# Kernel optimization log

Hardware: AMD Instinct MI355X
Metric: run time of the kernel (lower is better)

Reference implementation:

```python
import jax, jax.numpy as jnp
import numpy as np

INPUT_SHAPE = (4, 8, 8, 4)   # factorization of input_size=1024
RANK = 16                    # uniform TR rank; tr_ranks_line = [16]*9
NODES = 8                    # input_num=4, output_num=4
INPUT_NUM = 4


def setup_inputs() -> dict:
    key = jax.random.key(0)
    ks = jax.random.split(key, 10)
    B = 1024
    # node shapes from generate_node_shapes() with the chosen factorization
    node_shapes = [(256, 4), (16, 128), (16, 128), (16, 64),
                   (64, 16), (128, 16), (128, 16), (4, 256)]
    inp = {"x": jax.random.normal(ks[0], (B, 1024), dtype=jnp.float32)}
    for i, sh in enumerate(node_shapes):
        # kaiming_normal_(fan_in, linear) ~ N(0, sqrt(2/fan_in)) gain differences ignored for
        # correctness baseline; plain scaled normal init
        fan_in = sh[1]
        inp[f"node{i}"] = jax.random.normal(ks[i + 1], sh, dtype=jnp.float32) * np.float32(np.sqrt(1.0 / fan_in))
    inp["bias"] = jnp.zeros((1024,), dtype=jnp.float32)
    return inp


def _tensor_contract(x, weights):
    B = x.shape[0]
    # view(-1, *input_shape) then reverse the input mode axes (permute 0, n, n-1, ..., 1)
    res = x.reshape(B, *INPUT_SHAPE).transpose(0, 4, 3, 2, 1)  # (B, m3, m2, m1, m0)
    for i, W in enumerate(weights):
        wr = W.shape[1]
        if i == 0:
            res = res.reshape(-1, wr) @ W.T                 # (B*rest, r0*r1)
            res = res.reshape(B, -1, RANK).transpose(0, 2, 1)  # (B, r0, rest*r1)
        elif i < NODES - 1:
            # both remaining input nodes and all-but-last output nodes are a flat GEMM
            res = res.reshape(-1, wr) @ W.T
        else:
            # last node: (B, r_last_right, -1, r_last_left) -> swap ring ranks around middle
            res = res.reshape(B, RANK, -1, RANK).transpose(0, 2, 1, 3)
            res = res.reshape(-1, wr) @ W.T                 # (B*rest, m_last)
            res = res.reshape(B, -1)                         # (B, output_size)
    return res


def reference(x, node0, node1, node2, node3, node4, node5, node6, node7, bias):
    weights = [node0, node1, node2, node3, node4, node5, node6, node7]
    res = _tensor_contract(x, weights)
    return res + bias
```

## Files before the change

kernel.cpp:

```cpp
#include <hip/hip_runtime.h>
#include <hip/hip_bf16.h>

typedef __attribute__((ext_vector_type(8))) short bf16x8;
typedef __attribute__((ext_vector_type(4))) float f32x4;
typedef unsigned short u16;

static __device__ __forceinline__ u16 f2bf(float f) {
  unsigned u = __builtin_bit_cast(unsigned, f);
  return (u16)((u + 0x7fffu + ((u >> 16) & 1u)) >> 16);
}

__global__ __launch_bounds__(256) void trl_p1(
    const float* __restrict__ W0, const float* __restrict__ W1,
    const float* __restrict__ W2, const float* __restrict__ W3,
    const float* __restrict__ W4, const float* __restrict__ W5,
    const float* __restrict__ W6, const float* __restrict__ W7,
    const float* __restrict__ x,
    float* __restrict__ T1, float* __restrict__ V1,
    float* __restrict__ U1, float* __restrict__ V2,
    u16* __restrict__ xb) {
  const int gid = blockIdx.x * 256 + threadIdx.x;
  if (gid < 8192) {
    int i0 = gid & 3, i1 = (gid >> 2) & 7, j1 = (gid >> 5) & 15, r1 = gid >> 9;
    float s = 0.f;
#pragma unroll
    for (int r0 = 0; r0 < 16; ++r0)
      s += W1[j1 * 128 + i1 * 16 + r0] * W0[(r0 * 16 + r1) * 4 + i0];
    T1[gid] = s;
  } else if (gid < 16384) {
    int g = gid - 8192;
    int j1 = g & 15, i2 = (g >> 4) & 7, i3 = (g >> 7) & 3, j3 = g >> 9;
    float s = 0.f;
#pragma unroll
    for (int j2 = 0; j2 < 16; ++j2)
      s += W3[j3 * 64 + i3 * 16 + j2] * W2[j2 * 128 + i2 * 16 + j1];
    V1[g] = s;
  } else if (gid < 24576) {
    int g = gid - 16384;
    int j3 = g & 15, j5 = (g >> 4) & 127, kh = g >> 11;
    float s = 0.f;
#pragma unroll
    for (int kl = 0; kl < 16; ++kl)
      s += W5[j5 * 16 + kl] * W4[(kh * 16 + kl) * 16 + j3];
    U1[g] = s;
  } else {
    int g = gid - 24576;
    int j5l = g & 15, j6h = (g >> 4) & 7, r1 = (g >> 7) & 15, m7 = g >> 11;
    float s = 0.f;
#pragma unroll
    for (int d = 0; d < 16; ++d)
      s += W7[m7 * 256 + r1 * 16 + d] * W6[(j6h * 16 + d) * 16 + j5l];
    V2[g] = s;
  }
#pragma unroll
  for (int q = 0; q < 4; ++q) {
    const int c = gid + 65536 * q;
    const float4 v = reinterpret_cast<const float4*>(x)[c];
    ushort4 o4;
    o4.x = f2bf(v.x); o4.y = f2bf(v.y); o4.z = f2bf(v.z); o4.w = f2bf(v.w);
    reinterpret_cast<ushort4*>(xb)[c] = o4;
  }
}

__global__ __launch_bounds__(256) void trl_p2(
    const float* __restrict__ T1, const float* __restrict__ V1,
    const float* __restrict__ U1, const float* __restrict__ V2,
    u16* __restrict__ Apre, u16* __restrict__ Bmat) {
  const int gid = blockIdx.x * 256 + threadIdx.x;
  if (gid < 65536) {
    const int p = gid >> 8, irest = gid & 255;
    const int r1 = p >> 4, j3 = p & 15;
    const int i1 = irest >> 5, i2 = (irest >> 2) & 7, i3 = irest & 3;
    float4 a = make_float4(0.f, 0.f, 0.f, 0.f);
#pragma unroll
    for (int j1 = 0; j1 < 16; ++j1) {
      const float w = V1[((j3 * 4 + i3) * 8 + i2) * 16 + j1];
      const float4 t = reinterpret_cast<const float4*>(T1)[(r1 * 16 + j1) * 8 + i1];
      a.x += w * t.x; a.y += w * t.y; a.z += w * t.z; a.w += w * t.w;
    }
    Apre[p * 1024 + 0 * 256 + irest] = f2bf(a.x);
    Apre[p * 1024 + 1 * 256 + irest] = f2bf(a.y);
    Apre[p * 1024 + 2 * 256 + irest] = f2bf(a.z);
    Apre[p * 1024 + 3 * 256 + irest] = f2bf(a.w);
  } else {
    const int t = gid - 65536;
    const int o = t >> 6, rem = t & 63;
    const int r1 = rem >> 2, jq = rem & 3;
    const int m7 = o & 3, j6h = (o >> 2) & 7, j5h = (o >> 5) & 7, kh = o >> 8;
    float4 a = make_float4(0.f, 0.f, 0.f, 0.f);
#pragma unroll
    for (int j5l = 0; j5l < 16; ++j5l) {
      const float w = V2[((m7 * 16 + r1) * 8 + j6h) * 16 + j5l];
      const float4 u = reinterpret_cast<const float4*>(U1)[(kh * 128 + j5h * 16 + j5l) * 4 + jq];
      a.x += w * u.x; a.y += w * u.y; a.z += w * u.z; a.w += w * u.w;
    }
    ushort4 o4;
    o4.x = f2bf(a.x); o4.y = f2bf(a.y); o4.z = f2bf(a.z); o4.w = f2bf(a.w);
    *reinterpret_cast<ushort4*>(&Bmat[o * 256 + r1 * 16 + jq * 4]) = o4;
  }
}

__global__ __launch_bounds__(256) void trl_g1(const u16* __restrict__ A,
                                              const u16* __restrict__ B,
                                              u16* __restrict__ C) {
  __shared__ float red[3][32 * 33];
  const int tid = threadIdx.x;
  const int wave = tid >> 6, lane = tid & 63;
  const int l15 = lane & 15, l4 = lane >> 4;
  const int m0 = blockIdx.y * 32, n0 = blockIdx.x * 32;
  const int kbase = wave * 256;

  f32x4 acc[2][2] = {};
#pragma unroll
  for (int ks = 0; ks < 8; ++ks) {
    const int k = kbase + ks * 32 + l4 * 8;
    const bf16x8 a0 = *(const bf16x8*)&A[(size_t)(m0 + l15) * 1024 + k];
    const bf16x8 a1 = *(const bf16x8*)&A[(size_t)(m0 + 16 + l15) * 1024 + k];
    const bf16x8 b0 = *(const bf16x8*)&B[(size_t)(n0 + l15) * 1024 + k];
    const bf16x8 b1 = *(const bf16x8*)&B[(size_t)(n0 + 16 + l15) * 1024 + k];
    acc[0][0] = __builtin_amdgcn_mfma_f32_16x16x32_bf16(a0, b0, acc[0][0], 0, 0, 0);
    acc[0][1] = __builtin_amdgcn_mfma_f32_16x16x32_bf16(a0, b1, acc[0][1], 0, 0, 0);
    acc[1][0] = __builtin_amdgcn_mfma_f32_16x16x32_bf16(a1, b0, acc[1][0], 0, 0, 0);
    acc[1][1] = __builtin_amdgcn_mfma_f32_16x16x32_bf16(a1, b1, acc[1][1], 0, 0, 0);
  }

  if (wave > 0) {
#pragma unroll
    for (int fm = 0; fm < 2; ++fm)
#pragma unroll
      for (int fn = 0; fn < 2; ++fn)
#pragma unroll
        for (int r = 0; r < 4; ++r)
          red[wave - 1][(fm * 16 + l4 * 4 + r) * 33 + fn * 16 + l15] = acc[fm][fn][r];
  }
  __syncthreads();
  if (wave == 0) {
#pragma unroll
    for (int fm = 0; fm < 2; ++fm)
#pragma unroll
      for (int fn = 0; fn < 2; ++fn)
#pragma unroll
        for (int r = 0; r < 4; ++r) {
          const int row = fm * 16 + l4 * 4 + r, col = fn * 16 + l15;
          float s = acc[fm][fn][r] + red[0][row * 33 + col] + red[1][row * 33 + col] +
                    red[2][row * 33 + col];
          C[(size_t)(m0 + row) * 256 + n0 + col] = f2bf(s);
        }
  }
}

__global__ __launch_bounds__(256) void trl_g2(const u16* __restrict__ A,
                                              const u16* __restrict__ B,
                                              const float* __restrict__ bias,
                                              float* __restrict__ out) {
  const int tid = threadIdx.x;
  const int wave = tid >> 6, lane = tid & 63;
  const int l15 = lane & 15, l4 = lane >> 4;
  const int tile = blockIdx.x * 4 + wave;
  const int m0 = (tile >> 5) * 32, n0 = (tile & 31) * 32;

  f32x4 acc[2][2] = {};
#pragma unroll
  for (int ks = 0; ks < 8; ++ks) {
    const int k = ks * 32 + l4 * 8;
    const bf16x8 a0 = *(const bf16x8*)&A[(size_t)(m0 + l15) * 256 + k];
    const bf16x8 a1 = *(const bf16x8*)&A[(size_t)(m0 + 16 + l15) * 256 + k];
    const bf16x8 b0 = *(const bf16x8*)&B[(size_t)(n0 + l15) * 256 + k];
    const bf16x8 b1 = *(const bf16x8*)&B[(size_t)(n0 + 16 + l15) * 256 + k];
    acc[0][0] = __builtin_amdgcn_mfma_f32_16x16x32_bf16(a0, b0, acc[0][0], 0, 0, 0);
    acc[0][1] = __builtin_amdgcn_mfma_f32_16x16x32_bf16(a0, b1, acc[0][1], 0, 0, 0);
    acc[1][0] = __builtin_amdgcn_mfma_f32_16x16x32_bf16(a1, b0, acc[1][0], 0, 0, 0);
    acc[1][1] = __builtin_amdgcn_mfma_f32_16x16x32_bf16(a1, b1, acc[1][1], 0, 0, 0);
  }

#pragma unroll
  for (int fn = 0; fn < 2; ++fn) {
    const int gc = n0 + fn * 16 + l15;
    const float bv = bias[gc];
#pragma unroll
    for (int fm = 0; fm < 2; ++fm)
#pragma unroll
      for (int r = 0; r < 4; ++r) {
        const int gr = m0 + fm * 16 + l4 * 4 + r;
        out[(size_t)gr * 1024 + gc] = acc[fm][fn][r] + bv;
      }
  }
}

extern "C" void kernel_launch(void* const* d_in, const int* in_sizes, int n_in,
                              void* d_out, int out_size, void* d_ws, size_t ws_size,
                              hipStream_t stream) {
  const float* x  = (const float*)d_in[0];
  const float* W0 = (const float*)d_in[1];
  const float* W1 = (const float*)d_in[2];
  const float* W2 = (const float*)d_in[3];
  const float* W3 = (const float*)d_in[4];
  const float* W4 = (const float*)d_in[5];
  const float* W5 = (const float*)d_in[6];
  const float* W6 = (const float*)d_in[7];
  const float* W7 = (const float*)d_in[8];
  const float* bias = (const float*)d_in[9];

  char* ws = (char*)d_ws;
  float* T1 = (float*)(ws + (0 << 10));
  float* V1 = (float*)(ws + (32 << 10));
  float* U1 = (float*)(ws + (64 << 10));
  float* V2 = (float*)(ws + (96 << 10));
  u16* Apre = (u16*)(ws + (128 << 10));
  u16* Bmat = (u16*)(ws + (640 << 10));
  u16* xb   = (u16*)(ws + (1152 << 10));
  u16* Cb   = (u16*)(ws + (3200 << 10));
  float* outp = (float*)d_out;

  trl_p1<<<256, 256, 0, stream>>>(W0, W1, W2, W3, W4, W5, W6, W7, x, T1, V1, U1, V2, xb);
  trl_p2<<<512, 256, 0, stream>>>(T1, V1, U1, V2, Apre, Bmat);
  trl_g1<<<dim3(8, 32), 256, 0, stream>>>(xb, Apre, Cb);
  trl_g2<<<256, 256, 0, stream>>>(Cb, Bmat, bias, outp);
}
```

Before: 25.78 us.

## Fuse weight prep into one kernel and both GEMMs into one kernel

```diff
diff --git a/kernel.cpp b/kernel.cpp
--- a/kernel.cpp
+++ b/kernel.cpp
@@ -10,180 +10,156 @@
   return (u16)((u + 0x7fffu + ((u >> 16) & 1u)) >> 16);
 }
 
-__global__ __launch_bounds__(256) void trl_p1(
+__global__ __launch_bounds__(256) void trl_w(
     const float* __restrict__ W0, const float* __restrict__ W1,
     const float* __restrict__ W2, const float* __restrict__ W3,
     const float* __restrict__ W4, const float* __restrict__ W5,
     const float* __restrict__ W6, const float* __restrict__ W7,
-    const float* __restrict__ x,
-    float* __restrict__ T1, float* __restrict__ V1,
-    float* __restrict__ U1, float* __restrict__ V2,
-    u16* __restrict__ xb) {
-  const int gid = blockIdx.x * 256 + threadIdx.x;
-  if (gid < 8192) {
-    int i0 = gid & 3, i1 = (gid >> 2) & 7, j1 = (gid >> 5) & 15, r1 = gid >> 9;
-    float s = 0.f;
+    u16* __restrict__ Apre, u16* __restrict__ Bmat) {
+  __shared__ float S1[512];
+  __shared__ float S2[4096];
+  const int tid = threadIdx.x;
+  const int b = blockIdx.x;
+  if (b < 64) {
+    const int r1 = b >> 2;
+    const int j3base = (b & 3) << 2;
 #pragma unroll
-    for (int r0 = 0; r0 < 16; ++r0)
-      s += W1[j1 * 128 + i1 * 16 + r0] * W0[(r0 * 16 + r1) * 4 + i0];
-    T1[gid] = s;
-  } else if (gid < 16384) {
-    int g = gid - 8192;
-    int j1 = g & 15, i2 = (g >> 4) & 7, i3 = (g >> 7) & 3, j3 = g >> 9;
-    float s = 0.f;
+    for (int e0 = 0; e0 < 512; e0 += 256) {
+      const int e = e0 + tid;
+      const int i0 = e & 3, i1 = (e >> 2) & 7, j1 = e >> 5;
+      float s = 0.f;
 #pragma unroll
-    for (int j2 = 0; j2 < 16; ++j2)
-      s += W3[j3 * 64 + i3 * 16 + j2] * W2[j2 * 128 + i2 * 16 + j1];
-    V1[g] = s;
-  } else if (gid < 24576) {
-    int g = gid - 16384;
-    int j3 = g & 15, j5 = (g >> 4) & 127, kh = g >> 11;
-    float s = 0.f;
+      for (int r0 = 0; r0 < 16; ++r0)
+        s += W1[j1 * 128 + i1 * 16 + r0] * W0[(r0 * 16 + r1) * 4 + i0];
+      S1[e] = s;
+    }
 #pragma unroll
-    for (int kl = 0; kl < 16; ++kl)
-      s += W5[j5 * 16 + kl] * W4[(kh * 16 + kl) * 16 + j3];
-    U1[g] = s;
+    for (int e0 = 0; e0 < 2048; e0 += 256) {
+      const int e = e0 + tid;
+      const int i3 = e & 3, pd = (e >> 2) & 3, j1 = (e >> 4) & 15, i2 = e >> 8;
+      float s = 0.f;
+#pragma unroll
+      for (int j2 = 0; j2 < 16; ++j2)
+        s += W3[(j3base + pd) * 64 + i3 * 16 + j2] * W2[j2 * 128 + i2 * 16 + j1];
+      S2[e] = s;
+    }
+    __syncthreads();
+    const int i0 = tid & 3, i1 = (tid >> 2) & 7, i2 = tid >> 5;
+#pragma unroll
+    for (int pd = 0; pd < 4; ++pd) {
+      float a0 = 0.f, a1 = 0.f, a2 = 0.f, a3 = 0.f;
+#pragma unroll
+      for (int j1 = 0; j1 < 16; ++j1) {
+        const float t = S1[j1 * 32 + i1 * 4 + i0];
+        const float4 v = *(const float4*)&S2[i2 * 256 + j1 * 16 + pd * 4];
+        a0 += t * v.x; a1 += t * v.y; a2 += t * v.z; a3 += t * v.w;
+      }
+      ushort4 o4;
+      o4.x = f2bf(a0); o4.y = f2bf(a1); o4.z = f2bf(a2); o4.w = f2bf(a3);
+      *(ushort4*)&Apre[(size_t)(4 * b + pd) * 1024 + i0 * 256 + i1 * 32 + i2 * 4] = o4;
+    }
   } else {
-    int g = gid - 24576;
-    int j5l = g & 15, j6h = (g >> 4) & 7, r1 = (g >> 7) & 15, m7 = g >> 11;
-    float s = 0.f;
+    const int c = b - 64;
+    const int kh = c >> 4, j5h = (c >> 1) & 7, j6hbase = (c & 1) << 2;
+    {
+      const int j5l = tid >> 4, j3 = tid & 15;
+      float s = 0.f;
 #pragma unroll
-    for (int d = 0; d < 16; ++d)
-      s += W7[m7 * 256 + r1 * 16 + d] * W6[(j6h * 16 + d) * 16 + j5l];
-    V2[g] = s;
-  }
+      for (int kl = 0; kl < 16; ++kl)
+        s += W5[(j5h * 16 + j5l) * 16 + kl] * W4[(kh * 16 + kl) * 16 + j3];
+      S1[tid] = s;
+    }
 #pragma unroll
-  for (int q = 0; q < 4; ++q) {
-    const int c = gid + 65536 * q;
-    const float4 v = reinterpret_cast<const float4*>(x)[c];
-    ushort4 o4;
-    o4.x = f2bf(v.x); o4.y = f2bf(v.y); o4.z = f2bf(v.z); o4.w = f2bf(v.w);
-    reinterpret_cast<ushort4*>(xb)[c] = o4;
+    for (int e0 = 0; e0 < 4096; e0 += 256) {
+      const int e = e0 + tid;
+      const int j5l = e & 15, j6hd = (e >> 4) & 3, r1 = (e >> 6) & 15, m7 = e >> 10;
+      float s = 0.f;
+#pragma unroll
+      for (int d = 0; d < 16; ++d)
+        s += W7[m7 * 256 + r1 * 16 + d] * W6[((j6hbase + j6hd) * 16 + d) * 16 + j5l];
+      S2[e] = s;
+    }
+    __syncthreads();
+    const int r1 = (tid >> 2) & 15, j3q = tid & 3;
+#pragma unroll
+    for (int qq = 0; qq < 4; ++qq) {
+      const int od = qq * 4 + (tid >> 6);
+      const int m7 = od & 3, j6hd = od >> 2;
+      float a0 = 0.f, a1 = 0.f, a2 = 0.f, a3 = 0.f;
+#pragma unroll
+      for (int j5l = 0; j5l < 16; ++j5l) {
+        const float w = S2[((m7 * 16 + r1) * 4 + j6hd) * 16 + j5l];
+        const float4 u = *(const float4*)&S1[j5l * 16 + j3q * 4];
+        a0 += w * u.x; a1 += w * u.y; a2 += w * u.z; a3 += w * u.w;
+      }
+      ushort4 o4;
+      o4.x = f2bf(a0); o4.y = f2bf(a1); o4.z = f2bf(a2); o4.w = f2bf(a3);
+      *(ushort4*)&Bmat[(size_t)(16 * c + od) * 256 + r1 * 16 + j3q * 4] = o4;
+    }
   }
 }
 
-__global__ __launch_bounds__(256) void trl_p2(
-    const float* __restrict__ T1, const float* __restrict__ V1,
-    const float* __restrict__ U1, const float* __restrict__ V2,
-    u16* __restrict__ Apre, u16* __restrict__ Bmat) {
-  const int gid = blockIdx.x * 256 + threadIdx.x;
-  if (gid < 65536) {
-    const int p = gid >> 8, irest = gid & 255;
-    const int r1 = p >> 4, j3 = p & 15;
-    const int i1 = irest >> 5, i2 = (irest >> 2) & 7, i3 = irest & 3;
-    float4 a = make_float4(0.f, 0.f, 0.f, 0.f);
-#pragma unroll
-    for (int j1 = 0; j1 < 16; ++j1) {
-      const float w = V1[((j3 * 4 + i3) * 8 + i2) * 16 + j1];
-      const float4 t = reinterpret_cast<const float4*>(T1)[(r1 * 16 + j1) * 8 + i1];
-      a.x += w * t.x; a.y += w * t.y; a.z += w * t.z; a.w += w * t.w;
-    }
-    Apre[p * 1024 + 0 * 256 + irest] = f2bf(a.x);
-    Apre[p * 1024 + 1 * 256 + irest] = f2bf(a.y);
-    Apre[p * 1024 + 2 * 256 + irest] = f2bf(a.z);
-    Apre[p * 1024 + 3 * 256 + irest] = f2bf(a.w);
-  } else {
-    const int t = gid - 65536;
-    const int o = t >> 6, rem = t & 63;
-    const int r1 = rem >> 2, jq = rem & 3;
-    const int m7 = o & 3, j6h = (o >> 2) & 7, j5h = (o >> 5) & 7, kh = o >> 8;
-    float4 a = make_float4(0.f, 0.f, 0.f, 0.f);
-#pragma unroll
-    for (int j5l = 0; j5l < 16; ++j5l) {
-      const float w = V2[((m7 * 16 + r1) * 8 + j6h) * 16 + j5l];
-      const float4 u = reinterpret_cast<const float4*>(U1)[(kh * 128 + j5h * 16 + j5l) * 4 + jq];
-      a.x += w * u.x; a.y += w * u.y; a.z += w * u.z; a.w += w * u.w;
-    }
-    ushort4 o4;
-    o4.x = f2bf(a.x); o4.y = f2bf(a.y); o4.z = f2bf(a.z); o4.w = f2bf(a.w);
-    *reinterpret_cast<ushort4*>(&Bmat[o * 256 + r1 * 16 + jq * 4]) = o4;
-  }
-}
-
-__global__ __launch_bounds__(256) void trl_g1(const u16* __restrict__ A,
-                                              const u16* __restrict__ B,
-                                              u16* __restrict__ C) {
-  __shared__ float red[3][32 * 33];
+__global__ __launch_bounds__(256) void trl_g(const float* __restrict__ x,
+                                             const u16* __restrict__ Apre,
+                                             const u16* __restrict__ Bmat,
+                                             const float* __restrict__ bias,
+                                             float* __restrict__ out) {
+  __shared__ u16 Cbs[16 * 256];
   const int tid = threadIdx.x;
   const int wave = tid >> 6, lane = tid & 63;
   const int l15 = lane & 15, l4 = lane >> 4;
-  const int m0 = blockIdx.y * 32, n0 = blockIdx.x * 32;
-  const int kbase = wave * 256;
+  const int m0 = blockIdx.x * 16;
 
-  f32x4 acc[2][2] = {};
+  f32x4 acc1[4] = {};
+  {
+    const float* xrow = x + (size_t)(m0 + l15) * 1024;
+#pragma unroll 4
+    for (int kb = 0; kb < 32; ++kb) {
+      const int k = kb * 32 + l4 * 8;
+      const float4 f0 = *(const float4*)&xrow[k];
+      const float4 f1 = *(const float4*)&xrow[k + 4];
+      bf16x8 af;
+      af[0] = (short)f2bf(f0.x); af[1] = (short)f2bf(f0.y);
+      af[2] = (short)f2bf(f0.z); af[3] = (short)f2bf(f0.w);
+      af[4] = (short)f2bf(f1.x); af[5] = (short)f2bf(f1.y);
+      af[6] = (short)f2bf(f1.z); af[7] = (short)f2bf(f1.w);
 #pragma unroll
-  for (int ks = 0; ks < 8; ++ks) {
-    const int k = kbase + ks * 32 + l4 * 8;
-    const bf16x8 a0 = *(const bf16x8*)&A[(size_t)(m0 + l15) * 1024 + k];
-    const bf16x8 a1 = *(const bf16x8*)&A[(size_t)(m0 + 16 + l15) * 1024 + k];
-    const bf16x8 b0 = *(const bf16x8*)&B[(size_t)(n0 + l15) * 1024 + k];
-    const bf16x8 b1 = *(const bf16x8*)&B[(size_t)(n0 + 16 + l15) * 1024 + k];
-    acc[0][0] = __builtin_amdgcn_mfma_f32_16x16x32_bf16(a0, b0, acc[0][0], 0, 0, 0);
-    acc[0][1] = __builtin_amdgcn_mfma_f32_16x16x32_bf16(a0, b1, acc[0][1], 0, 0, 0);
-    acc[1][0] = __builtin_amdgcn_mfma_f32_16x16x32_bf16(a1, b0, acc[1][0], 0, 0, 0);
-    acc[1][1] = __builtin_amdgcn_mfma_f32_16x16x32_bf16(a1, b1, acc[1][1], 0, 0, 0);
+      for (int nt = 0; nt < 4; ++nt) {
+        const bf16x8 bf = *(const bf16x8*)&Apre[(size_t)(wave * 64 + nt * 16 + l15) * 1024 + k];
+        acc1[nt] = __builtin_amdgcn_mfma_f32_16x16x32_bf16(af, bf, acc1[nt], 0, 0, 0);
+      }
+    }
   }
-
-  if (wave > 0) {
 #pragma unroll
-    for (int fm = 0; fm < 2; ++fm)
+  for (int nt = 0; nt < 4; ++nt) {
+    const int col = wave * 64 + nt * 16 + l15;
 #pragma unroll
-      for (int fn = 0; fn < 2; ++fn)
-#pragma unroll
-        for (int r = 0; r < 4; ++r)
-          red[wave - 1][(fm * 16 + l4 * 4 + r) * 33 + fn * 16 + l15] = acc[fm][fn][r];
+    for (int r = 0; r < 4; ++r) {
+      const int row = l4 * 4 + r;
+      Cbs[row * 256 + ((((col >> 3) ^ (row & 7)) << 3) | (col & 7))] = f2bf(acc1[nt][r]);
+    }
   }
   __syncthreads();
-  if (wave == 0) {
+
+  f32x4 acc2[16] = {};
+#pragma unroll 2
+  for (int kb = 0; kb < 8; ++kb) {
+    const int g = kb * 4 + l4;
+    const bf16x8 af = *(const bf16x8*)&Cbs[l15 * 256 + ((g ^ (l15 & 7)) << 3)];
 #pragma unroll
-    for (int fm = 0; fm < 2; ++fm)
+    for (int nt = 0; nt < 16; ++nt) {
+      const bf16x8 bf =
+          *(const bf16x8*)&Bmat[(size_t)(wave * 256 + nt * 16 + l15) * 256 + kb * 32 + l4 * 8];
+      acc2[nt] = __builtin_amdgcn_mfma_f32_16x16x32_bf16(af, bf, acc2[nt], 0, 0, 0);
+    }
+  }
 #pragma unroll
-      for (int fn = 0; fn < 2; ++fn)
+  for (int nt = 0; nt < 16; ++nt) {
+    const int col = wave * 256 + nt * 16 + l15;
+    const float bv = bias[col];
 #pragma unroll
-        for (int r = 0; r < 4; ++r) {
-          const int row = fm * 16 + l4 * 4 + r, col = fn * 16 + l15;
-          float s = acc[fm][fn][r] + red[0][row * 33 + col] + red[1][row * 33 + col] +
-                    red[2][row * 33 + col];
-          C[(size_t)(m0 + row) * 256 + n0 + col] = f2bf(s);
-        }
-  }
-}
-
-__global__ __launch_bounds__(256) void trl_g2(const u16* __restrict__ A,
-                                              const u16* __restrict__ B,
-                                              const float* __restrict__ bias,
-                                              float* __restrict__ out) {
-  const int tid = threadIdx.x;
-  const int wave = tid >> 6, lane = tid & 63;
-  const int l15 = lane & 15, l4 = lane >> 4;
-  const int tile = blockIdx.x * 4 + wave;
-  const int m0 = (tile >> 5) * 32, n0 = (tile & 31) * 32;
-
-  f32x4 acc[2][2] = {};
-#pragma unroll
-  for (int ks = 0; ks < 8; ++ks) {
-    const int k = ks * 32 + l4 * 8;
-    const bf16x8 a0 = *(const bf16x8*)&A[(size_t)(m0 + l15) * 256 + k];
-    const bf16x8 a1 = *(const bf16x8*)&A[(size_t)(m0 + 16 + l15) * 256 + k];
-    const bf16x8 b0 = *(const bf16x8*)&B[(size_t)(n0 + l15) * 256 + k];
-    const bf16x8 b1 = *(const bf16x8*)&B[(size_t)(n0 + 16 + l15) * 256 + k];
-    acc[0][0] = __builtin_amdgcn_mfma_f32_16x16x32_bf16(a0, b0, acc[0][0], 0, 0, 0);
-    acc[0][1] = __builtin_amdgcn_mfma_f32_16x16x32_bf16(a0, b1, acc[0][1], 0, 0, 0);
-    acc[1][0] = __builtin_amdgcn_mfma_f32_16x16x32_bf16(a1, b0, acc[1][0], 0, 0, 0);
-    acc[1][1] = __builtin_amdgcn_mfma_f32_16x16x32_bf16(a1, b1, acc[1][1], 0, 0, 0);
-  }
-
-#pragma unroll
-  for (int fn = 0; fn < 2; ++fn) {
-    const int gc = n0 + fn * 16 + l15;
-    const float bv = bias[gc];
-#pragma unroll
-    for (int fm = 0; fm < 2; ++fm)
-#pragma unroll
-      for (int r = 0; r < 4; ++r) {
-        const int gr = m0 + fm * 16 + l4 * 4 + r;
-        out[(size_t)gr * 1024 + gc] = acc[fm][fn][r] + bv;
-      }
+    for (int r = 0; r < 4; ++r)
+      out[(size_t)(m0 + l4 * 4 + r) * 1024 + col] = acc2[nt][r] + bv;
   }
 }
 
@@ -202,18 +178,10 @@
   const float* bias = (const float*)d_in[9];
 
   char* ws = (char*)d_ws;
-  float* T1 = (float*)(ws + (0 << 10));
-  float* V1 = (float*)(ws + (32 << 10));
-  float* U1 = (float*)(ws + (64 << 10));
-  float* V2 = (float*)(ws + (96 << 10));
-  u16* Apre = (u16*)(ws + (128 << 10));
-  u16* Bmat = (u16*)(ws + (640 << 10));
-  u16* xb   = (u16*)(ws + (1152 << 10));
-  u16* Cb   = (u16*)(ws + (3200 << 10));
+  u16* Apre = (u16*)(ws);
+  u16* Bmat = (u16*)(ws + (512 << 10));
   float* outp = (float*)d_out;
 
-  trl_p1<<<256, 256, 0, stream>>>(W0, W1, W2, W3, W4, W5, W6, W7, x, T1, V1, U1, V2, xb);
-  trl_p2<<<512, 256, 0, stream>>>(T1, V1, U1, V2, Apre, Bmat);
-  trl_g1<<<dim3(8, 32), 256, 0, stream>>>(xb, Apre, Cb);
-  trl_g2<<<256, 256, 0, stream>>>(Cb, Bmat, bias, outp);
+  trl_w<<<128, 256, 0, stream>>>(W0, W1, W2, W3, W4, W5, W6, W7, Apre, Bmat);
+  trl_g<<<64, 256, 0, stream>>>(x, Apre, Bmat, bias, outp);
 }
```

Result: slower. 72.78 us (+182.3%).

## Fuse weight-contraction prologues into GEMM kernels, building B tiles in LDS

Applied to the files above, without the earlier changes.

```diff
diff --git a/kernel.cpp b/kernel.cpp
--- a/kernel.cpp
+++ b/kernel.cpp
@@ -10,120 +10,95 @@
   return (u16)((u + 0x7fffu + ((u >> 16) & 1u)) >> 16);
 }
 
-__global__ __launch_bounds__(256) void trl_p1(
+__global__ __launch_bounds__(256) void trl_g1(
+    const float* __restrict__ x,
     const float* __restrict__ W0, const float* __restrict__ W1,
     const float* __restrict__ W2, const float* __restrict__ W3,
-    const float* __restrict__ W4, const float* __restrict__ W5,
-    const float* __restrict__ W6, const float* __restrict__ W7,
-    const float* __restrict__ x,
-    float* __restrict__ T1, float* __restrict__ V1,
-    float* __restrict__ U1, float* __restrict__ V2,
-    u16* __restrict__ xb) {
-  const int gid = blockIdx.x * 256 + threadIdx.x;
-  if (gid < 8192) {
-    int i0 = gid & 3, i1 = (gid >> 2) & 7, j1 = (gid >> 5) & 15, r1 = gid >> 9;
+    u16* __restrict__ Cb) {
+  __shared__ float S_T1[1024];
+  __shared__ float S_V1[8192];
+  __shared__ u16 Bs[128 * 32 * 8];
+  __shared__ float red[3][32 * 33];
+  const int tid = threadIdx.x;
+  const int n0 = blockIdx.x * 32;
+  const int m0 = blockIdx.y * 32;
+  const int r1a = n0 >> 4;
+
+  for (int k = 0; k < 4; ++k) {
+    const int e = tid + 256 * k;
+    const int i0 = e & 3, i1 = (e >> 2) & 7, j1 = (e >> 5) & 15, rr = e >> 9;
     float s = 0.f;
 #pragma unroll
     for (int r0 = 0; r0 < 16; ++r0)
-      s += W1[j1 * 128 + i1 * 16 + r0] * W0[(r0 * 16 + r1) * 4 + i0];
-    T1[gid] = s;
-  } else if (gid < 16384) {
-    int g = gid - 8192;
-    int j1 = g & 15, i2 = (g >> 4) & 7, i3 = (g >> 7) & 3, j3 = g >> 9;
+      s += W1[j1 * 128 + i1 * 16 + r0] * W0[(r0 * 16 + r1a + rr) * 4 + i0];
+    S_T1[e] = s;
+  }
+  for (int k = 0; k < 32; ++k) {
+    const int e = tid + 256 * k;
+    const int j1 = e & 15, i2 = (e >> 4) & 7, i3 = (e >> 7) & 3, j3 = e >> 9;
     float s = 0.f;
 #pragma unroll
     for (int j2 = 0; j2 < 16; ++j2)
       s += W3[j3 * 64 + i3 * 16 + j2] * W2[j2 * 128 + i2 * 16 + j1];
-    V1[g] = s;
-  } else if (gid < 24576) {
-    int g = gid - 16384;
-    int j3 = g & 15, j5 = (g >> 4) & 127, kh = g >> 11;
-    float s = 0.f;
-#pragma unroll
-    for (int kl = 0; kl < 16; ++kl)
-      s += W5[j5 * 16 + kl] * W4[(kh * 16 + kl) * 16 + j3];
-    U1[g] = s;
-  } else {
-    int g = gid - 24576;
-    int j5l = g & 15, j6h = (g >> 4) & 7, r1 = (g >> 7) & 15, m7 = g >> 11;
-    float s = 0.f;
-#pragma unroll
-    for (int d = 0; d < 16; ++d)
-      s += W7[m7 * 256 + r1 * 16 + d] * W6[(j6h * 16 + d) * 16 + j5l];
-    V2[g] = s;
-  }
-#pragma unroll
-  for (int q = 0; q < 4; ++q) {
-    const int c = gid + 65536 * q;
-    const float4 v = reinterpret_cast<const float4*>(x)[c];
-    ushort4 o4;
-    o4.x = f2bf(v.x); o4.y = f2bf(v.y); o4.z = f2bf(v.z); o4.w = f2bf(v.w);
-    reinterpret_cast<ushort4*>(xb)[c] = o4;
-  }
-}
-
-__global__ __launch_bounds__(256) void trl_p2(
-    const float* __restrict__ T1, const float* __restrict__ V1,
-    const float* __restrict__ U1, const float* __restrict__ V2,
-    u16* __restrict__ Apre, u16* __restrict__ Bmat) {
-  const int gid = blockIdx.x * 256 + threadIdx.x;
-  if (gid < 65536) {
-    const int p = gid >> 8, irest = gid & 255;
-    const int r1 = p >> 4, j3 = p & 15;
-    const int i1 = irest >> 5, i2 = (irest >> 2) & 7, i3 = irest & 3;
-    float4 a = make_float4(0.f, 0.f, 0.f, 0.f);
-#pragma unroll
-    for (int j1 = 0; j1 < 16; ++j1) {
-      const float w = V1[((j3 * 4 + i3) * 8 + i2) * 16 + j1];
-      const float4 t = reinterpret_cast<const float4*>(T1)[(r1 * 16 + j1) * 8 + i1];
-      a.x += w * t.x; a.y += w * t.y; a.z += w * t.z; a.w += w * t.w;
+    S_V1[e] = s;
+  }
+  __syncthreads();
+
+  for (int tau = 0; tau < 16; ++tau) {
+    const int q = (tid & 7) + 8 * (tau >> 2);
+    const int grp = (tid >> 3) * 4 + (tau & 3);
+    const int i0 = grp >> 5, i1 = (grp >> 2) & 7, gg = grp & 3;
+    const int rr = q >> 4, j3 = q & 15;
+    float tq[16];
+#pragma unroll
+    for (int j1 = 0; j1 < 16; ++j1) tq[j1] = S_T1[rr * 512 + j1 * 32 + i1 * 4 + i0];
+    float a[8];
+#pragma unroll
+    for (int s = 0; s < 8; ++s) {
+      const int i2 = gg * 2 + (s >> 2), i3 = s & 3;
+      const float* vp = &S_V1[j3 * 512 + i3 * 128 + i2 * 16];
+      float acc = 0.f;
+#pragma unroll
+      for (int j1 = 0; j1 < 16; ++j1) acc += tq[j1] * vp[j1];
+      a[s] = acc;
     }
-    Apre[p * 1024 + 0 * 256 + irest] = f2bf(a.x);
-    Apre[p * 1024 + 1 * 256 + irest] = f2bf(a.y);
-    Apre[p * 1024 + 2 * 256 + irest] = f2bf(a.z);
-    Apre[p * 1024 + 3 * 256 + irest] = f2bf(a.w);
-  } else {
-    const int t = gid - 65536;
-    const int o = t >> 6, rem = t & 63;
-    const int r1 = rem >> 2, jq = rem & 3;
-    const int m7 = o & 3, j6h = (o >> 2) & 7, j5h = (o >> 5) & 7, kh = o >> 8;
-    float4 a = make_float4(0.f, 0.f, 0.f, 0.f);
-#pragma unroll
-    for (int j5l = 0; j5l < 16; ++j5l) {
-      const float w = V2[((m7 * 16 + r1) * 8 + j6h) * 16 + j5l];
-      const float4 u = reinterpret_cast<const float4*>(U1)[(kh * 128 + j5h * 16 + j5l) * 4 + jq];
-      a.x += w * u.x; a.y += w * u.y; a.z += w * u.z; a.w += w * u.w;
-    }
-    ushort4 o4;
-    o4.x = f2bf(a.x); o4.y = f2bf(a.y); o4.z = f2bf(a.z); o4.w = f2bf(a.w);
-    *reinterpret_cast<ushort4*>(&Bmat[o * 256 + r1 * 16 + jq * 4]) = o4;
-  }
-}
-
-__global__ __launch_bounds__(256) void trl_g1(const u16* __restrict__ A,
-                                              const u16* __restrict__ B,
-                                              u16* __restrict__ C) {
-  __shared__ float red[3][32 * 33];
-  const int tid = threadIdx.x;
+    bf16x8 w;
+#pragma unroll
+    for (int s = 0; s < 8; ++s) w[s] = (short)f2bf(a[s]);
+    const int granule = i0 * 32 + i1 * 4 + gg;
+    *(bf16x8*)&Bs[(granule * 32 + q) * 8] = w;
+  }
+  __syncthreads();
+
   const int wave = tid >> 6, lane = tid & 63;
   const int l15 = lane & 15, l4 = lane >> 4;
-  const int m0 = blockIdx.y * 32, n0 = blockIdx.x * 32;
-  const int kbase = wave * 256;
-
   f32x4 acc[2][2] = {};
+  const float* xr0 = x + (size_t)(m0 + l15) * 1024;
+  const float* xr1 = x + (size_t)(m0 + 16 + l15) * 1024;
 #pragma unroll
   for (int ks = 0; ks < 8; ++ks) {
-    const int k = kbase + ks * 32 + l4 * 8;
-    const bf16x8 a0 = *(const bf16x8*)&A[(size_t)(m0 + l15) * 1024 + k];
-    const bf16x8 a1 = *(const bf16x8*)&A[(size_t)(m0 + 16 + l15) * 1024 + k];
-    const bf16x8 b0 = *(const bf16x8*)&B[(size_t)(n0 + l15) * 1024 + k];
-    const bf16x8 b1 = *(const bf16x8*)&B[(size_t)(n0 + 16 + l15) * 1024 + k];
+    const int k = wave * 256 + ks * 32 + l4 * 8;
+    const float4 f0 = *(const float4*)&xr0[k];
+    const float4 f1 = *(const float4*)&xr0[k + 4];
+    const float4 g0 = *(const float4*)&xr1[k];
+    const float4 g1 = *(const float4*)&xr1[k + 4];
+    bf16x8 a0, a1;
+    a0[0] = (short)f2bf(f0.x); a0[1] = (short)f2bf(f0.y);
+    a0[2] = (short)f2bf(f0.z); a0[3] = (short)f2bf(f0.w);
+    a0[4] = (short)f2bf(f1.x); a0[5] = (short)f2bf(f1.y);
+    a0[6] = (short)f2bf(f1.z); a0[7] = (short)f2bf(f1.w);
+    a1[0] = (short)f2bf(g0.x); a1[1] = (short)f2bf(g0.y);
+    a1[2] = (short)f2bf(g0.z); a1[3] = (short)f2bf(g0.w);
+    a1[4] = (short)f2bf(g1.x); a1[5] = (short)f2bf(g1.y);
+    a1[6] = (short)f2bf(g1.z); a1[7] = (short)f2bf(g1.w);
+    const int kg = wave * 32 + ks * 4 + l4;
+    const bf16x8 b0 = *(const bf16x8*)&Bs[(kg * 32 + l15) * 8];
+    const bf16x8 b1 = *(const bf16x8*)&Bs[(kg * 32 + 16 + l15) * 8];
     acc[0][0] = __builtin_amdgcn_mfma_f32_16x16x32_bf16(a0, b0, acc[0][0], 0, 0, 0);
     acc[0][1] = __builtin_amdgcn_mfma_f32_16x16x32_bf16(a0, b1, acc[0][1], 0, 0, 0);
     acc[1][0] = __builtin_amdgcn_mfma_f32_16x16x32_bf16(a1, b0, acc[1][0], 0, 0, 0);
     acc[1][1] = __builtin_amdgcn_mfma_f32_16x16x32_bf16(a1, b1, acc[1][1], 0, 0, 0);
   }
-
   if (wave > 0) {
 #pragma unroll
     for (int fm = 0; fm < 2; ++fm)
@@ -144,38 +119,90 @@
           const int row = fm * 16 + l4 * 4 + r, col = fn * 16 + l15;
           float s = acc[fm][fn][r] + red[0][row * 33 + col] + red[1][row * 33 + col] +
                     red[2][row * 33 + col];
-          C[(size_t)(m0 + row) * 256 + n0 + col] = f2bf(s);
+          Cb[(size_t)(m0 + row) * 256 + n0 + col] = f2bf(s);
         }
   }
 }
 
-__global__ __launch_bounds__(256) void trl_g2(const u16* __restrict__ A,
-                                              const u16* __restrict__ B,
-                                              const float* __restrict__ bias,
-                                              float* __restrict__ out) {
+__global__ __launch_bounds__(256) void trl_g2(
+    const u16* __restrict__ Cb,
+    const float* __restrict__ W4, const float* __restrict__ W5,
+    const float* __restrict__ W6, const float* __restrict__ W7,
+    const float* __restrict__ bias,
+    float* __restrict__ out) {
+  __shared__ float S_U1[4 * 256];
+  __shared__ float S_V2[8192];
+  __shared__ u16 Bs[32 * 128 * 8];
   const int tid = threadIdx.x;
+  const int B7 = blockIdx.x;
+  const int nb = B7 * 128;
+  const int m0 = blockIdx.y * 32;
+  const int kh = B7 >> 1;
+
+  for (int k = 0; k < 4; ++k) {
+    const int j5l = tid >> 4, j3 = tid & 15;
+    const int j5h = (4 * B7 + k) & 7;
+    float s = 0.f;
+#pragma unroll
+    for (int kl = 0; kl < 16; ++kl)
+      s += W5[(j5h * 16 + j5l) * 16 + kl] * W4[(kh * 16 + kl) * 16 + j3];
+    S_U1[k * 256 + tid] = s;
+  }
+  for (int k = 0; k < 32; ++k) {
+    const int e = tid + 256 * k;
+    const int j5l = e & 15, j6h = (e >> 4) & 7, r1 = (e >> 7) & 15, m7 = e >> 11;
+    float s = 0.f;
+#pragma unroll
+    for (int d = 0; d < 16; ++d)
+      s += W7[m7 * 256 + r1 * 16 + d] * W6[(j6h * 16 + d) * 16 + j5l];
+    S_V2[e] = s;
+  }
+  __syncthreads();
+
+  for (int tau = 0; tau < 16; ++tau) {
+    const int ol = (tid & 7) + 8 * (tau & 7) + 64 * (tid >> 7);
+    const int rj = ((tid >> 3) & 15) * 2 + (tau >> 3);
+    const int r1 = rj >> 1, j3h = rj & 1;
+    const int m7 = ol & 3, j6hd = (ol >> 2) & 3;
+    const int j6h = ((ol >> 4) & 1) * 4 + j6hd;
+    const int cslot = ol >> 5;
+    const float* vp = &S_V2[((m7 * 16 + r1) * 8 + j6h) * 16];
+    const float* up = &S_U1[cslot * 256 + j3h * 8];
+    float a[8] = {};
+#pragma unroll
+    for (int j5l = 0; j5l < 16; ++j5l) {
+      const float v = vp[j5l];
+      const float* u = &up[j5l * 16];
+#pragma unroll
+      for (int s = 0; s < 8; ++s) a[s] += v * u[s];
+    }
+    bf16x8 w;
+#pragma unroll
+    for (int s = 0; s < 8; ++s) w[s] = (short)f2bf(a[s]);
+    const int granule = r1 * 2 + j3h;
+    *(bf16x8*)&Bs[(granule * 128 + ol) * 8] = w;
+  }
+  __syncthreads();
+
   const int wave = tid >> 6, lane = tid & 63;
   const int l15 = lane & 15, l4 = lane >> 4;
-  const int tile = blockIdx.x * 4 + wave;
-  const int m0 = (tile >> 5) * 32, n0 = (tile & 31) * 32;
-
   f32x4 acc[2][2] = {};
 #pragma unroll
   for (int ks = 0; ks < 8; ++ks) {
     const int k = ks * 32 + l4 * 8;
-    const bf16x8 a0 = *(const bf16x8*)&A[(size_t)(m0 + l15) * 256 + k];
-    const bf16x8 a1 = *(const bf16x8*)&A[(size_t)(m0 + 16 + l15) * 256 + k];
-    const bf16x8 b0 = *(const bf16x8*)&B[(size_t)(n0 + l15) * 256 + k];
-    const bf16x8 b1 = *(const bf16x8*)&B[(size_t)(n0 + 16 + l15) * 256 + k];
+    const bf16x8 a0 = *(const bf16x8*)&Cb[(size_t)(m0 + l15) * 256 + k];
+    const bf16x8 a1 = *(const bf16x8*)&Cb[(size_t)(m0 + 16 + l15) * 256 + k];
+    const int kg = ks * 4 + l4;
+    const bf16x8 b0 = *(const bf16x8*)&Bs[(kg * 128 + wave * 32 + l15) * 8];
+    const bf16x8 b1 = *(const bf16x8*)&Bs[(kg * 128 + wave * 32 + 16 + l15) * 8];
     acc[0][0] = __builtin_amdgcn_mfma_f32_16x16x32_bf16(a0, b0, acc[0][0], 0, 0, 0);
     acc[0][1] = __builtin_amdgcn_mfma_f32_16x16x32_bf16(a0, b1, acc[0][1], 0, 0, 0);
     acc[1][0] = __builtin_amdgcn_mfma_f32_16x16x32_bf16(a1, b0, acc[1][0], 0, 0, 0);
     acc[1][1] = __builtin_amdgcn_mfma_f32_16x16x32_bf16(a1, b1, acc[1][1], 0, 0, 0);
   }
-
 #pragma unroll
   for (int fn = 0; fn < 2; ++fn) {
-    const int gc = n0 + fn * 16 + l15;
+    const int gc = nb + wave * 32 + fn * 16 + l15;
     const float bv = bias[gc];
 #pragma unroll
     for (int fm = 0; fm < 2; ++fm)
@@ -202,18 +229,9 @@
   const float* bias = (const float*)d_in[9];
 
   char* ws = (char*)d_ws;
-  float* T1 = (float*)(ws + (0 << 10));
-  float* V1 = (float*)(ws + (32 << 10));
-  float* U1 = (float*)(ws + (64 << 10));
-  float* V2 = (float*)(ws + (96 << 10));
-  u16* Apre = (u16*)(ws + (128 << 10));
-  u16* Bmat = (u16*)(ws + (640 << 10));
-  u16* xb   = (u16*)(ws + (1152 << 10));
-  u16* Cb   = (u16*)(ws + (3200 << 10));
+  u16* Cb = (u16*)ws;
   float* outp = (float*)d_out;
 
-  trl_p1<<<256, 256, 0, stream>>>(W0, W1, W2, W3, W4, W5, W6, W7, x, T1, V1, U1, V2, xb);
-  trl_p2<<<512, 256, 0, stream>>>(T1, V1, U1, V2, Apre, Bmat);
-  trl_g1<<<dim3(8, 32), 256, 0, stream>>>(xb, Apre, Cb);
-  trl_g2<<<256, 256, 0, stream>>>(Cb, Bmat, bias, outp);
-}
+  trl_g1<<<dim3(8, 32), 256, 0, stream>>>(x, W0, W1, W2, W3, Cb);
+  trl_g2<<<dim3(8, 32), 256, 0, stream>>>(Cb, W4, W5, W6, W7, bias, outp);
+}
```

New measurement: 86.21 us. +234.3%, slower.
